# Performance work log

Measured on AMD Instinct MI355X. Metric: run time of the kernel, lower is better.

The kernel has to match this reference:

```python
import jax, jax.numpy as jnp
import numpy as np
from jax import lax

STRIDES = (4, 8, 16, 32, 64)
SIZES = (32, 64, 128, 256, 512)
RATIOS = (0.5, 1.0, 2.0)
IMG_H, IMG_W = 1024, 1024
PRE_NMS = 1000
POST_NMS = 1000
NMS_THRESH = 0.7
BBOX_CLIP = float(np.log(1000.0 / 16.0))
NEG_INF = -1e9


def _cell_anchors(size):
    a = []
    for r in RATIOS:
        w = size * np.sqrt(1.0 / r)
        h = size * np.sqrt(r)
        a.append([-w / 2.0, -h / 2.0, w / 2.0, h / 2.0])
    return np.array(a, np.float32)  # [A,4]


def _level_anchors(H, W, stride, size):
    cell = _cell_anchors(size)  # [A,4]
    ys = np.arange(H, dtype=np.float32) * stride
    xs = np.arange(W, dtype=np.float32) * stride
    yy, xx = np.meshgrid(ys, xs, indexing='ij')  # row-major (H,W)
    shifts = np.stack([xx, yy, xx, yy], axis=-1).reshape(-1, 1, 4)
    return jnp.asarray((shifts + cell[None]).reshape(-1, 4))  # [(H*W*A),4] in (H,W,A) order


def conv2d(x, w, b, pad):
    y = lax.conv_general_dilated(x, w, (1, 1), pad,
                                 dimension_numbers=('NCHW', 'OIHW', 'NCHW'))
    return y + b[None, :, None, None]


def decode(deltas, anchors):
    widths = anchors[:, 2] - anchors[:, 0] + 1.0
    heights = anchors[:, 3] - anchors[:, 1] + 1.0
    ctr_x = anchors[:, 0] + 0.5 * widths
    ctr_y = anchors[:, 1] + 0.5 * heights
    dx, dy = deltas[..., 0], deltas[..., 1]
    dw = jnp.minimum(deltas[..., 2], BBOX_CLIP)
    dh = jnp.minimum(deltas[..., 3], BBOX_CLIP)
    pcx = dx * widths + ctr_x
    pcy = dy * heights + ctr_y
    pw = jnp.exp(dw) * widths
    ph = jnp.exp(dh) * heights
    return jnp.stack([pcx - 0.5 * pw, pcy - 0.5 * ph,
                      pcx + 0.5 * pw - 1.0, pcy + 0.5 * ph - 1.0], axis=-1)


def iou_matrix(boxes):
    area = (boxes[:, 2] - boxes[:, 0]) * (boxes[:, 3] - boxes[:, 1])
    lt = jnp.maximum(boxes[:, None, :2], boxes[None, :, :2])
    rb = jnp.minimum(boxes[:, None, 2:], boxes[None, :, 2:])
    wh = jnp.maximum(rb - lt, 0.0)
    inter = wh[..., 0] * wh[..., 1]
    return inter / (area[:, None] + area[None, :] - inter + 1e-9)


def nms_keep(boxes):
    # boxes [N,4] already sorted by score desc; greedy NMS -> bool keep mask
    N = boxes.shape[0]
    iou = iou_matrix(boxes)

    def body(keep, i):
        row = jnp.take(iou, i, axis=0) > NMS_THRESH
        row = row.at[i].set(False)
        keep = jnp.where(keep[i], keep & ~row, keep)
        return keep, None

    keep, _ = lax.scan(body, jnp.ones((N,), bool), jnp.arange(N))
    return keep


def _forward(feats, conv_w, conv_b, cls_w, cls_b, bbox_w, bbox_b):
    level_boxes, level_scores = [], []
    for lvl, feat in enumerate(feats):
        B, _, H, W = feat.shape
        t = jax.nn.relu(conv2d(feat, conv_w, conv_b, 'SAME'))
        logits = conv2d(t, cls_w, cls_b, 'VALID')    # [B,A,H,W]
        breg = conv2d(t, bbox_w, bbox_b, 'VALID')    # [B,4A,H,W]
        A = logits.shape[1]
        scores = jnp.transpose(logits, (0, 2, 3, 1)).reshape(B, -1)            # (H,W,A)
        deltas = breg.reshape(B, A, 4, H, W).transpose(0, 3, 4, 1, 2).reshape(B, -1, 4)
        anchors = _level_anchors(H, W, STRIDES[lvl], SIZES[lvl])
        boxes = decode(deltas, anchors)  # [B,N,4]
        boxes = jnp.stack([jnp.clip(boxes[..., 0], 0.0, IMG_W - 1.0),
                           jnp.clip(boxes[..., 1], 0.0, IMG_H - 1.0),
                           jnp.clip(boxes[..., 2], 0.0, IMG_W - 1.0),
                           jnp.clip(boxes[..., 3], 0.0, IMG_H - 1.0)], axis=-1)
        k = min(PRE_NMS, scores.shape[1])
        top_s, idx = lax.top_k(scores, k)                                   # [B,k]
        top_b = jnp.take_along_axis(boxes, idx[..., None], axis=1)          # [B,k,4]
        keep = jax.vmap(nms_keep)(top_b)                                    # [B,k] bool
        level_scores.append(jnp.where(keep, top_s, NEG_INF))
        level_boxes.append(top_b)
    all_s = jnp.concatenate(level_scores, axis=1)
    all_b = jnp.concatenate(level_boxes, axis=1)
    fs, fi = lax.top_k(all_s, POST_NMS)                                     # [B,POST]
    fb = jnp.take_along_axis(all_b, fi[..., None], axis=1)                  # [B,POST,4]
    return jnp.concatenate([fb, fs[..., None]], axis=-1)                    # [B,POST,5]


def setup_inputs() -> dict:
    key = jax.random.key(0)
    ks = jax.random.split(key, 8)
    C = 256
    feats = {
        'feat0': jax.random.normal(ks[0], (2, C, 256, 256), jnp.float32),
        'feat1': jax.random.normal(ks[1], (2, C, 128, 128), jnp.float32),
        'feat2': jax.random.normal(ks[2], (2, C, 64, 64), jnp.float32),
        'feat3': jax.random.normal(ks[3], (2, C, 32, 32), jnp.float32),
        'feat4': jax.random.normal(ks[4], (2, C, 16, 16), jnp.float32),
    }
    params = {
        'conv_w': jax.random.normal(ks[5], (C, C, 3, 3), jnp.float32) * 0.01,
        'conv_b': jnp.zeros((C,), jnp.float32),
        'cls_w': jax.random.normal(ks[6], (3, C, 1, 1), jnp.float32) * 0.01,
        'cls_b': jnp.zeros((3,), jnp.float32),
        'bbox_w': jax.random.normal(ks[7], (12, C, 1, 1), jnp.float32) * 0.01,
        'bbox_b': jnp.zeros((12,), jnp.float32),
    }
    return {**feats, **params}


def reference(feat0, feat1, feat2, feat3, feat4, conv_w, conv_b, cls_w, cls_b, bbox_w, bbox_b):
    return _forward([feat0, feat1, feat2, feat3, feat4],
                    conv_w, conv_b, cls_w, cls_b, bbox_w, bbox_b)
```

## Files before the change

### kernel.cpp

```cpp
#include <hip/hip_runtime.h>
#include <cmath>


#define NTOT_PER_IMG 261888
#define ATOT_PER_IMG 4768

__constant__ int c_NLVL[5] = {196608, 49152, 12288, 3072, 768};
__constant__ int c_KLVL[5] = {1000, 1000, 1000, 1000, 768};
__constant__ int c_LOFF[5] = {0, 196608, 245760, 258048, 261120};
__constant__ int c_AOFF[5] = {0, 1000, 2000, 3000, 4000};

struct Anch { float cx1[3]; float cy1[3]; };
struct ConvCfg { Anch an[5]; };

__global__ __launch_bounds__(256) void wtrans(const float* __restrict__ Wsrc,
                                              float* __restrict__ Wt) {
  __shared__ float T[16][17];
  int k0 = blockIdx.x * 16;
  int o0 = blockIdx.y * 16;
  int i = threadIdx.x >> 4, j = threadIdx.x & 15;
  T[i][j] = Wsrc[(size_t)(o0 + i) * 2304 + (k0 + j)];
  __syncthreads();
  Wt[(size_t)(k0 + i) * 256 + (o0 + j)] = T[j][i];
}

__global__ __launch_bounds__(256, 6) void conv_all(
    const float* __restrict__ f0, const float* __restrict__ f1,
    const float* __restrict__ f2, const float* __restrict__ f3,
    const float* __restrict__ f4, const float* __restrict__ Wt,
    const float* __restrict__ convb, const float* __restrict__ clsw,
    const float* __restrict__ clsb, const float* __restrict__ bboxw,
    const float* __restrict__ bboxb, float* __restrict__ scoresOut,
    float4* __restrict__ boxesOut, ConvCfg cfg) {
  __shared__ __align__(16) float sm[4096 + 272];
  float* tl = sm;
  float* Red2 = sm + 4096;

  int b = blockIdx.x;
  const float* feat;
  int lvl, img, gy, bx, H, stride, lvlOff;
  if (b < 8192) {
    lvl = 0; feat = f0; H = 256; stride = 4; lvlOff = 0;
    img = b >> 12; int r = b & 4095; gy = r >> 4; bx = r & 15;
  } else if (b < 10240) {
    lvl = 1; feat = f1; H = 128; stride = 8; lvlOff = 196608;
    int rb = b - 8192; img = rb >> 10; int r = rb & 1023; gy = r >> 3; bx = r & 7;
  } else if (b < 10752) {
    lvl = 2; feat = f2; H = 64; stride = 16; lvlOff = 245760;
    int rb = b - 10240; img = rb >> 8; int r = rb & 255; gy = r >> 2; bx = r & 3;
  } else if (b < 10880) {
    lvl = 3; feat = f3; H = 32; stride = 32; lvlOff = 258048;
    int rb = b - 10752; img = rb >> 6; int r = rb & 63; gy = r >> 1; bx = r & 1;
  } else {
    lvl = 4; feat = f4; H = 16; stride = 64; lvlOff = 261120;
    int rb = b - 10880; img = rb >> 4; gy = rb & 15; bx = 0;
  }
  const int W = H;
  const int x0 = bx * 16;
  const Anch an = cfg.an[lvl];

  const int tid = threadIdx.x;
  const int lane = tid & 63;
  const int wav = __builtin_amdgcn_readfirstlane(tid >> 6);
  const int oc = wav * 64 + lane;

  const float* f = feat + (size_t)img * 256 * H * W;

  float acc[16];
#pragma unroll
  for (int p = 0; p < 16; p++) acc[p] = 0.f;

  const bool leftEdge = (x0 == 0);
  const bool rightEdge = (x0 + 16 >= W);

#pragma unroll 1
  for (int ic = 0; ic < 256; ic++) {
    const float* frow0 = f + (size_t)ic * H * W;
#pragma unroll
    for (int ky = 0; ky < 3; ky++) {
      int row = gy + ky - 1;
      float a[18];
      if (row >= 0 && row < H) {
        const float* rp = frow0 + (size_t)row * W + x0;
#pragma unroll
        for (int j = 0; j < 16; j++) a[j + 1] = rp[j];
        a[0] = leftEdge ? 0.f : rp[-1];
        a[17] = rightEdge ? 0.f : rp[16];
      } else {
#pragma unroll
        for (int j = 0; j < 18; j++) a[j] = 0.f;
      }
      const float* wrow = Wt + (size_t)(ic * 9 + ky * 3) * 256 + oc;
      float w0 = wrow[0];
      float w1 = wrow[256];
      float w2 = wrow[512];
#pragma unroll
      for (int p = 0; p < 16; p++) acc[p] = __builtin_fmaf(w0, a[p], acc[p]);
#pragma unroll
      for (int p = 0; p < 16; p++) acc[p] = __builtin_fmaf(w1, a[p + 1], acc[p]);
#pragma unroll
      for (int p = 0; p < 16; p++) acc[p] = __builtin_fmaf(w2, a[p + 2], acc[p]);
    }
  }

  float cb = convb[oc];
#pragma unroll
  for (int p = 0; p < 16; p++)
    tl[p * 256 + oc] = fmaxf(acc[p] + cb, 0.f);
  __syncthreads();

  if (tid < 240) {
    int px = tid / 15, c = tid - px * 15;
    const float* wr0 = (c < 3) ? (clsw + c * 256) : (bboxw + (c - 3) * 256);
    float bb = (c < 3) ? clsb[c] : bboxb[c - 3];
    const float* trow = &tl[px * 256];
    float tot = 0.f;
#pragma unroll
    for (int g = 0; g < 16; g++) {
      const float* wr = wr0 + g * 16;
      const float* tr = trow + g * 16;
      float s = 0.f;
#pragma unroll
      for (int i = 0; i < 16; i++) s += wr[i] * tr[i];
      tot += s;
    }
    Red2[px * 17 + c] = tot + bb;
  }
  __syncthreads();

  const float BCLIP = (float)4.135166556742356;
  const size_t base = (size_t)img * NTOT_PER_IMG + lvlOff;
  if (tid < 48) {
    int px = tid / 3, a = tid - px * 3;
    int gx = x0 + px;
    float sc = Red2[px * 17 + a];
    float dxv = Red2[px * 17 + 3 + a * 4 + 0];
    float dyv = Red2[px * 17 + 3 + a * 4 + 1];
    float dwv = Red2[px * 17 + 3 + a * 4 + 2];
    float dhv = Red2[px * 17 + 3 + a * 4 + 3];
    float sx = (float)(gx * stride), sy = (float)(gy * stride);
    float x1 = __fadd_rn(sx, an.cx1[a]);
    float x2 = __fsub_rn(sx, an.cx1[a]);
    float y1 = __fadd_rn(sy, an.cy1[a]);
    float y2 = __fsub_rn(sy, an.cy1[a]);
    float wdt = __fadd_rn(__fsub_rn(x2, x1), 1.0f);
    float hgt = __fadd_rn(__fsub_rn(y2, y1), 1.0f);
    float ctx = __fadd_rn(x1, __fmul_rn(0.5f, wdt));
    float cty = __fadd_rn(y1, __fmul_rn(0.5f, hgt));
    float dw = fminf(dwv, BCLIP), dh = fminf(dhv, BCLIP);
    float pcx = __fadd_rn(__fmul_rn(dxv, wdt), ctx);
    float pcy = __fadd_rn(__fmul_rn(dyv, hgt), cty);
    float pw = __fmul_rn(expf(dw), wdt);
    float ph = __fmul_rn(expf(dh), hgt);
    float hw = __fmul_rn(0.5f, pw), hh = __fmul_rn(0.5f, ph);
    float bx1 = __fsub_rn(pcx, hw);
    float by1 = __fsub_rn(pcy, hh);
    float bx2 = __fsub_rn(__fadd_rn(pcx, hw), 1.0f);
    float by2 = __fsub_rn(__fadd_rn(pcy, hh), 1.0f);
    bx1 = fminf(fmaxf(bx1, 0.f), 1023.f);
    by1 = fminf(fmaxf(by1, 0.f), 1023.f);
    bx2 = fminf(fmaxf(bx2, 0.f), 1023.f);
    by2 = fminf(fmaxf(by2, 0.f), 1023.f);
    int g = gy * W + gx;
    size_t o = base + (size_t)g * 3 + a;
    scoresOut[o] = sc;
    boxesOut[o] = make_float4(bx1, by1, bx2, by2);
  }
}

__device__ __forceinline__ unsigned fkey(float f) {
  unsigned b = __float_as_uint(f);
  return (b & 0x80000000u) ? ~b : (b | 0x80000000u);
}
__device__ __forceinline__ float funkey(unsigned u) {
  unsigned b = (u & 0x80000000u) ? (u & 0x7fffffffu) : ~u;
  return __uint_as_float(b);
}

template <bool FINAL>
__global__ __launch_bounds__(1024) void topk_kernel(
    const float* __restrict__ scoresIn, const float4* __restrict__ boxesIn,
    float* __restrict__ scoresOut, float4* __restrict__ boxesOut,
    float* __restrict__ finalOut) {
  __shared__ unsigned long long keys[1024];
  __shared__ unsigned hist[256];
  __shared__ unsigned s_comm[4];
  int lvl = 0, img, N, k;
  const float* src;
  const float4* bsrc;
  if (FINAL) {
    img = blockIdx.x; N = ATOT_PER_IMG; k = 1000;
    src = scoresIn + (size_t)img * ATOT_PER_IMG;
    bsrc = boxesIn + (size_t)img * ATOT_PER_IMG;
  } else {
    lvl = blockIdx.x; img = blockIdx.y;
    N = c_NLVL[lvl]; k = c_KLVL[lvl];
    src = scoresIn + (size_t)img * NTOT_PER_IMG + c_LOFF[lvl];
    bsrc = boxesIn + (size_t)img * NTOT_PER_IMG + c_LOFF[lvl];
  }
  const int tid = threadIdx.x;

  unsigned pref = 0, pmask = 0, krem = (unsigned)k, cntT = 0;
  for (int pass = 3; pass >= 0; pass--) {
    int shift = pass * 8;
    if (tid < 256) hist[tid] = 0;
    __syncthreads();
    for (int i = tid; i < N; i += 1024) {
      unsigned u = fkey(src[i]);
      if ((u & pmask) == pref) atomicAdd(&hist[(u >> shift) & 255], 1u);
    }
    __syncthreads();
    if (tid == 0) {
      unsigned cum = 0;
      for (int d = 255; d >= 0; d--) {
        unsigned c = hist[d];
        if (cum + c >= krem) {
          s_comm[0] = krem - cum; s_comm[1] = c; s_comm[2] = (unsigned)d;
          break;
        }
        cum += c;
      }
    }
    __syncthreads();
    krem = s_comm[0]; cntT = s_comm[1];
    pref |= s_comm[2] << shift;
    pmask |= 0xFFu << shift;
    __syncthreads();
  }
  const unsigned T = pref, r = krem;
  unsigned m = (unsigned)N;
  if (r < cntT) {
    unsigned lo = 0, hi = (unsigned)N;
    while (lo < hi) {
      unsigned mid = (lo + hi) >> 1;
      if (tid == 0) s_comm[3] = 0;
      __syncthreads();
      for (unsigned i = tid; i < mid; i += 1024)
        if (fkey(src[i]) == T) atomicAdd(&s_comm[3], 1u);
      __syncthreads();
      unsigned c = s_comm[3];
      __syncthreads();
      if (c >= r) hi = mid; else lo = mid + 1;
    }
    m = lo;
  }
  if (tid == 0) s_comm[3] = 0;
  __syncthreads();
  for (int i = tid; i < N; i += 1024) {
    unsigned u = fkey(src[i]);
    if (u > T || (u == T && (unsigned)i < m)) {
      unsigned p = atomicAdd(&s_comm[3], 1u);
      if (p < 1024)
        keys[p] = ((unsigned long long)u << 32) | (unsigned)(~(unsigned)i);
    }
  }
  __syncthreads();
  if (tid >= k) keys[tid] = 0ull;
  __syncthreads();
  for (unsigned k2 = 2; k2 <= 1024; k2 <<= 1) {
    for (unsigned j = k2 >> 1; j > 0; j >>= 1) {
      unsigned i = tid, ixj = i ^ j;
      if (ixj > i) {
        unsigned long long a = keys[i], b = keys[ixj];
        bool sw = ((i & k2) == 0) ? (a < b) : (a > b);
        if (sw) { keys[i] = b; keys[ixj] = a; }
      }
      __syncthreads();
    }
  }
  if (tid < k) {
    unsigned long long key = keys[tid];
    unsigned u = (unsigned)(key >> 32);
    unsigned idx = ~((unsigned)key);
    float sc = funkey(u);
    float4 b = bsrc[idx];
    if (FINAL) {
      float* o = finalOut + ((size_t)img * 1000 + tid) * 5;
      o[0] = b.x; o[1] = b.y; o[2] = b.z; o[3] = b.w; o[4] = sc;
    } else {
      scoresOut[(size_t)img * ATOT_PER_IMG + c_AOFF[lvl] + tid] = sc;
      boxesOut[(size_t)img * ATOT_PER_IMG + c_AOFF[lvl] + tid] = b;
    }
  }
}

__global__ __launch_bounds__(256) void nms_matrix(
    const float4* __restrict__ allb, unsigned long long* __restrict__ supp) {
  int lvl = blockIdx.x, img = blockIdx.y, rb = blockIdx.z;
  int k = c_KLVL[lvl];
  int task = img * 5 + lvl;
  const float4* src = allb + (size_t)img * ATOT_PER_IMG + c_AOFF[lvl];
  __shared__ float4 bb[1000];
  __shared__ float ar[1000];
  for (int j = threadIdx.x; j < k; j += 256) {
    float4 b = src[j];
    bb[j] = b;
    ar[j] = __fmul_rn(__fsub_rn(b.z, b.x), __fsub_rn(b.w, b.y));
  }
  __syncthreads();
  int i = rb * 256 + threadIdx.x;
  if (i < k) {
    float4 bi = bb[i];
    float ai = ar[i];
    unsigned long long* row = supp + ((size_t)task * 1024 + i) * 16;
    int jw0 = i >> 6;
    for (int jw = 0; jw < jw0; jw++) row[jw] = 0ull;
    for (int jw = jw0; jw < 16; jw++) {
      unsigned long long bits = 0;
      int jbase = jw * 64;
      for (int jj = 0; jj < 64; jj++) {
        int j = jbase + jj;
        if (j > i && j < k) {
          float4 bj = bb[j];
          float ltx = fmaxf(bi.x, bj.x), lty = fmaxf(bi.y, bj.y);
          float rbx = fminf(bi.z, bj.z), rby = fminf(bi.w, bj.w);
          float wx = fmaxf(__fsub_rn(rbx, ltx), 0.f);
          float wy = fmaxf(__fsub_rn(rby, lty), 0.f);
          float inter = __fmul_rn(wx, wy);
          float den = __fadd_rn(__fsub_rn(__fadd_rn(ai, ar[j]), inter), 1e-9f);
          if (__fdiv_rn(inter, den) > 0.7f) bits |= 1ull << jj;
        }
      }
      row[jw] = bits;
    }
  }
}

__global__ __launch_bounds__(64) void nms_scan(
    const float* __restrict__ topS, const unsigned long long* __restrict__ supp,
    float* __restrict__ fscore) {
  int lvl = blockIdx.x, img = blockIdx.y;
  int k = c_KLVL[lvl];
  int task = img * 5 + lvl;
  int lane = threadIdx.x;
  const unsigned long long* base = supp + (size_t)task * 1024 * 16;
  unsigned long long rem = 0, keep = 0;
  for (int b0 = 0; b0 < k; b0 += 16) {
    unsigned long long buf[16];
#pragma unroll
    for (int t = 0; t < 16; t++) {
      int i = b0 + t;
      buf[t] = (lane < 16 && i < k) ? base[(size_t)i * 16 + lane] : 0ull;
    }
#pragma unroll
    for (int t = 0; t < 16; t++) {
      int i = b0 + t;
      if (i >= k) break;
      int wi = i >> 6, bi = i & 63;
      unsigned long long rw = __shfl(rem, wi);
      if (!((rw >> bi) & 1ull)) {
        rem |= buf[t];
        if (lane == wi) keep |= (1ull << bi);
      }
    }
  }
  const float* ts = topS + (size_t)img * ATOT_PER_IMG + c_AOFF[lvl];
  float* fs = fscore + (size_t)img * ATOT_PER_IMG + c_AOFF[lvl];
  for (int i = lane; i < k; i += 64) {
    int wi = i >> 6;
    unsigned long long kw = __shfl(keep, wi);
    fs[i] = ((kw >> (i & 63)) & 1ull) ? ts[i] : -1e9f;
  }
}

static Anch mkAnch(double size) {
  Anch a;
  const double R[3] = {0.5, 1.0, 2.0};
  for (int i = 0; i < 3; i++) {
    double w = size * sqrt(1.0 / R[i]);
    double h = size * sqrt(R[i]);
    a.cx1[i] = (float)(-w / 2.0);
    a.cy1[i] = (float)(-h / 2.0);
  }
  return a;
}

extern "C" void kernel_launch(void* const* d_in, const int* in_sizes, int n_in,
                              void* d_out, int out_size, void* d_ws,
                              size_t ws_size, hipStream_t stream) {
  (void)in_sizes; (void)n_in; (void)out_size; (void)ws_size;
  const float* f0 = (const float*)d_in[0];
  const float* f1 = (const float*)d_in[1];
  const float* f2 = (const float*)d_in[2];
  const float* f3 = (const float*)d_in[3];
  const float* f4 = (const float*)d_in[4];
  const float* conv_w = (const float*)d_in[5];
  const float* conv_b = (const float*)d_in[6];
  const float* cls_w  = (const float*)d_in[7];
  const float* cls_b  = (const float*)d_in[8];
  const float* bbox_w = (const float*)d_in[9];
  const float* bbox_b = (const float*)d_in[10];
  float* out = (float*)d_out;

  float* wsf = (float*)d_ws;
  float* Wt     = wsf;
  float* scores = Wt + 589824;
  float* boxes  = scores + 2 * NTOT_PER_IMG;
  float* topS   = boxes + (size_t)2 * NTOT_PER_IMG * 4;
  float* allb   = topS + 2 * ATOT_PER_IMG;
  float* fscore = allb + (size_t)2 * ATOT_PER_IMG * 4;
  unsigned long long* supp =
      (unsigned long long*)(fscore + 2 * ATOT_PER_IMG);

  wtrans<<<dim3(144, 16), 256, 0, stream>>>(conv_w, Wt);

  ConvCfg cfg;
  const double SZ[5] = {32, 64, 128, 256, 512};
  for (int l = 0; l < 5; l++) cfg.an[l] = mkAnch(SZ[l]);

  conv_all<<<10912, 256, 0, stream>>>(f0, f1, f2, f3, f4, Wt, conv_b, cls_w,
                                      cls_b, bbox_w, bbox_b, scores,
                                      (float4*)boxes, cfg);

  topk_kernel<false><<<dim3(5, 2), 1024, 0, stream>>>(
      scores, (const float4*)boxes, topS, (float4*)allb, nullptr);
  nms_matrix<<<dim3(5, 2, 4), 256, 0, stream>>>((const float4*)allb, supp);
  nms_scan<<<dim3(5, 2), 64, 0, stream>>>(topS, supp, fscore);
  topk_kernel<true><<<2, 1024, 0, stream>>>(
      fscore, (const float4*)allb, nullptr, nullptr, out);
}
```

Measured before the change: 3.827 ms.

## Compute two output rows per conv block to reuse loaded input rows and weights

Each conv block now produces two adjacent output rows. It loads four input rows per channel instead of three per output row, and loads all nine weights once for both rows, which halves the grid. Out-of-bounds rows are now handled with clamped addresses and bit masks instead of branches. The cost is twice the accumulator registers, which may reduce occupancy under the 6-wave launch bound, and the head/decode epilogue now runs twice per block with extra barriers.

```diff
diff --git a/kernel.cpp b/kernel.cpp
--- a/kernel.cpp
+++ b/kernel.cpp
@@ -38,25 +38,27 @@
 
   int b = blockIdx.x;
   const float* feat;
-  int lvl, img, gy, bx, H, stride, lvlOff;
-  if (b < 8192) {
+  int lvl, img, gy2, bx, H, stride, lvlOff;
+  if (b < 4096) {
     lvl = 0; feat = f0; H = 256; stride = 4; lvlOff = 0;
-    img = b >> 12; int r = b & 4095; gy = r >> 4; bx = r & 15;
-  } else if (b < 10240) {
+    img = b >> 11; int r = b & 2047; gy2 = r >> 4; bx = r & 15;
+  } else if (b < 5120) {
     lvl = 1; feat = f1; H = 128; stride = 8; lvlOff = 196608;
-    int rb = b - 8192; img = rb >> 10; int r = rb & 1023; gy = r >> 3; bx = r & 7;
-  } else if (b < 10752) {
+    int rb = b - 4096; img = rb >> 9; int r = rb & 511; gy2 = r >> 3; bx = r & 7;
+  } else if (b < 5376) {
     lvl = 2; feat = f2; H = 64; stride = 16; lvlOff = 245760;
-    int rb = b - 10240; img = rb >> 8; int r = rb & 255; gy = r >> 2; bx = r & 3;
-  } else if (b < 10880) {
+    int rb = b - 5120; img = rb >> 7; int r = rb & 127; gy2 = r >> 2; bx = r & 3;
+  } else if (b < 5440) {
     lvl = 3; feat = f3; H = 32; stride = 32; lvlOff = 258048;
-    int rb = b - 10752; img = rb >> 6; int r = rb & 63; gy = r >> 1; bx = r & 1;
+    int rb = b - 5376; img = rb >> 5; int r = rb & 31; gy2 = r >> 1; bx = r & 1;
   } else {
     lvl = 4; feat = f4; H = 16; stride = 64; lvlOff = 261120;
-    int rb = b - 10880; img = rb >> 4; gy = rb & 15; bx = 0;
+    int rb = b - 5440; img = rb >> 3; gy2 = rb & 7; bx = 0;
   }
   const int W = H;
+  const int HW = H * W;
   const int x0 = bx * 16;
+  const int gy0 = gy2 * 2;
   const Anch an = cfg.an[lvl];
 
   const int tid = threadIdx.x;
@@ -64,107 +66,135 @@
   const int wav = __builtin_amdgcn_readfirstlane(tid >> 6);
   const int oc = wav * 64 + lane;
 
-  const float* f = feat + (size_t)img * 256 * H * W;
-
-  float acc[16];
-#pragma unroll
-  for (int p = 0; p < 16; p++) acc[p] = 0.f;
+  const float* f = feat + (size_t)img * 256 * HW;
+
+  float acc0[16], acc1[16];
+#pragma unroll
+  for (int p = 0; p < 16; p++) { acc0[p] = 0.f; acc1[p] = 0.f; }
 
   const bool leftEdge = (x0 == 0);
   const bool rightEdge = (x0 + 16 >= W);
+  const unsigned mskL = leftEdge ? 0u : 0xFFFFFFFFu;
+  const unsigned mskR = rightEdge ? 0u : 0xFFFFFFFFu;
+  const int offL = leftEdge ? 0 : -1;
+  const int offR = rightEdge ? 15 : 16;
+
+#define LOADROW(arr, rowi)                                                   \
+  {                                                                          \
+    int row_ = (rowi);                                                       \
+    unsigned msk_ = (row_ >= 0 && row_ < H) ? 0xFFFFFFFFu : 0u;              \
+    int rc_ = row_ < 0 ? 0 : (row_ >= H ? H - 1 : row_);                     \
+    const float* rp_ = pl + (size_t)rc_ * W + x0;                            \
+    arr[0] = __uint_as_float(__float_as_uint(rp_[offL]) & msk_ & mskL);      \
+    _Pragma("unroll")                                                        \
+    for (int j_ = 0; j_ < 16; j_++)                                          \
+      arr[j_ + 1] = __uint_as_float(__float_as_uint(rp_[j_]) & msk_);        \
+    arr[17] = __uint_as_float(__float_as_uint(rp_[offR]) & msk_ & mskR);     \
+  }
+
+#define FMA3(accA, arr, w0_, w1_, w2_)                                       \
+  {                                                                          \
+    _Pragma("unroll")                                                        \
+    for (int p_ = 0; p_ < 16; p_++)                                          \
+      accA[p_] = __builtin_fmaf(w0_, arr[p_], accA[p_]);                     \
+    _Pragma("unroll")                                                        \
+    for (int p_ = 0; p_ < 16; p_++)                                          \
+      accA[p_] = __builtin_fmaf(w1_, arr[p_ + 1], accA[p_]);                 \
+    _Pragma("unroll")                                                        \
+    for (int p_ = 0; p_ < 16; p_++)                                          \
+      accA[p_] = __builtin_fmaf(w2_, arr[p_ + 2], accA[p_]);                 \
+  }
 
 #pragma unroll 1
   for (int ic = 0; ic < 256; ic++) {
-    const float* frow0 = f + (size_t)ic * H * W;
-#pragma unroll
-    for (int ky = 0; ky < 3; ky++) {
-      int row = gy + ky - 1;
-      float a[18];
-      if (row >= 0 && row < H) {
-        const float* rp = frow0 + (size_t)row * W + x0;
-#pragma unroll
-        for (int j = 0; j < 16; j++) a[j + 1] = rp[j];
-        a[0] = leftEdge ? 0.f : rp[-1];
-        a[17] = rightEdge ? 0.f : rp[16];
-      } else {
-#pragma unroll
-        for (int j = 0; j < 18; j++) a[j] = 0.f;
-      }
-      const float* wrow = Wt + (size_t)(ic * 9 + ky * 3) * 256 + oc;
-      float w0 = wrow[0];
-      float w1 = wrow[256];
-      float w2 = wrow[512];
-#pragma unroll
-      for (int p = 0; p < 16; p++) acc[p] = __builtin_fmaf(w0, a[p], acc[p]);
-#pragma unroll
-      for (int p = 0; p < 16; p++) acc[p] = __builtin_fmaf(w1, a[p + 1], acc[p]);
-#pragma unroll
-      for (int p = 0; p < 16; p++) acc[p] = __builtin_fmaf(w2, a[p + 2], acc[p]);
-    }
-  }
-
-  float cb = convb[oc];
-#pragma unroll
-  for (int p = 0; p < 16; p++)
-    tl[p * 256 + oc] = fmaxf(acc[p] + cb, 0.f);
-  __syncthreads();
-
-  if (tid < 240) {
-    int px = tid / 15, c = tid - px * 15;
-    const float* wr0 = (c < 3) ? (clsw + c * 256) : (bboxw + (c - 3) * 256);
-    float bb = (c < 3) ? clsb[c] : bboxb[c - 3];
-    const float* trow = &tl[px * 256];
-    float tot = 0.f;
-#pragma unroll
-    for (int g = 0; g < 16; g++) {
-      const float* wr = wr0 + g * 16;
-      const float* tr = trow + g * 16;
-      float s = 0.f;
-#pragma unroll
-      for (int i = 0; i < 16; i++) s += wr[i] * tr[i];
-      tot += s;
-    }
-    Red2[px * 17 + c] = tot + bb;
-  }
-  __syncthreads();
-
+    const float* pl = f + (size_t)ic * HW;
+    const float* wrow = Wt + (size_t)ic * 9 * 256 + oc;
+    float w00 = wrow[0 * 256], w01 = wrow[1 * 256], w02 = wrow[2 * 256];
+    float w10 = wrow[3 * 256], w11 = wrow[4 * 256], w12 = wrow[5 * 256];
+    float w20 = wrow[6 * 256], w21 = wrow[7 * 256], w22 = wrow[8 * 256];
+    float R0[18], R1[18], R2[18], R3[18];
+    LOADROW(R0, gy0 - 1)
+    LOADROW(R1, gy0)
+    LOADROW(R2, gy0 + 1)
+    LOADROW(R3, gy0 + 2)
+    FMA3(acc0, R0, w00, w01, w02)
+    FMA3(acc1, R1, w00, w01, w02)
+    FMA3(acc0, R1, w10, w11, w12)
+    FMA3(acc1, R2, w10, w11, w12)
+    FMA3(acc0, R2, w20, w21, w22)
+    FMA3(acc1, R3, w20, w21, w22)
+  }
+#undef LOADROW
+#undef FMA3
+
+  const float cb = convb[oc];
   const float BCLIP = (float)4.135166556742356;
   const size_t base = (size_t)img * NTOT_PER_IMG + lvlOff;
-  if (tid < 48) {
-    int px = tid / 3, a = tid - px * 3;
-    int gx = x0 + px;
-    float sc = Red2[px * 17 + a];
-    float dxv = Red2[px * 17 + 3 + a * 4 + 0];
-    float dyv = Red2[px * 17 + 3 + a * 4 + 1];
-    float dwv = Red2[px * 17 + 3 + a * 4 + 2];
-    float dhv = Red2[px * 17 + 3 + a * 4 + 3];
-    float sx = (float)(gx * stride), sy = (float)(gy * stride);
-    float x1 = __fadd_rn(sx, an.cx1[a]);
-    float x2 = __fsub_rn(sx, an.cx1[a]);
-    float y1 = __fadd_rn(sy, an.cy1[a]);
-    float y2 = __fsub_rn(sy, an.cy1[a]);
-    float wdt = __fadd_rn(__fsub_rn(x2, x1), 1.0f);
-    float hgt = __fadd_rn(__fsub_rn(y2, y1), 1.0f);
-    float ctx = __fadd_rn(x1, __fmul_rn(0.5f, wdt));
-    float cty = __fadd_rn(y1, __fmul_rn(0.5f, hgt));
-    float dw = fminf(dwv, BCLIP), dh = fminf(dhv, BCLIP);
-    float pcx = __fadd_rn(__fmul_rn(dxv, wdt), ctx);
-    float pcy = __fadd_rn(__fmul_rn(dyv, hgt), cty);
-    float pw = __fmul_rn(expf(dw), wdt);
-    float ph = __fmul_rn(expf(dh), hgt);
-    float hw = __fmul_rn(0.5f, pw), hh = __fmul_rn(0.5f, ph);
-    float bx1 = __fsub_rn(pcx, hw);
-    float by1 = __fsub_rn(pcy, hh);
-    float bx2 = __fsub_rn(__fadd_rn(pcx, hw), 1.0f);
-    float by2 = __fsub_rn(__fadd_rn(pcy, hh), 1.0f);
-    bx1 = fminf(fmaxf(bx1, 0.f), 1023.f);
-    by1 = fminf(fmaxf(by1, 0.f), 1023.f);
-    bx2 = fminf(fmaxf(bx2, 0.f), 1023.f);
-    by2 = fminf(fmaxf(by2, 0.f), 1023.f);
-    int g = gy * W + gx;
-    size_t o = base + (size_t)g * 3 + a;
-    scoresOut[o] = sc;
-    boxesOut[o] = make_float4(bx1, by1, bx2, by2);
+
+#pragma unroll
+  for (int rr = 0; rr < 2; rr++) {
+    const int gy = gy0 + rr;
+#pragma unroll
+    for (int p = 0; p < 16; p++)
+      tl[p * 256 + oc] = fmaxf((rr ? acc1[p] : acc0[p]) + cb, 0.f);
+    __syncthreads();
+
+    if (tid < 240) {
+      int px = tid / 15, c = tid - px * 15;
+      const float* wr0 = (c < 3) ? (clsw + c * 256) : (bboxw + (c - 3) * 256);
+      float bb = (c < 3) ? clsb[c] : bboxb[c - 3];
+      const float* trow = &tl[px * 256];
+      float tot = 0.f;
+#pragma unroll
+      for (int g = 0; g < 16; g++) {
+        const float* wr = wr0 + g * 16;
+        const float* tr = trow + g * 16;
+        float s = 0.f;
+#pragma unroll
+        for (int i = 0; i < 16; i++) s += wr[i] * tr[i];
+        tot += s;
+      }
+      Red2[px * 17 + c] = tot + bb;
+    }
+    __syncthreads();
+
+    if (tid < 48) {
+      int px = tid / 3, a = tid - px * 3;
+      int gx = x0 + px;
+      float sc = Red2[px * 17 + a];
+      float dxv = Red2[px * 17 + 3 + a * 4 + 0];
+      float dyv = Red2[px * 17 + 3 + a * 4 + 1];
+      float dwv = Red2[px * 17 + 3 + a * 4 + 2];
+      float dhv = Red2[px * 17 + 3 + a * 4 + 3];
+      float sx = (float)(gx * stride), sy = (float)(gy * stride);
+      float x1 = __fadd_rn(sx, an.cx1[a]);
+      float x2 = __fsub_rn(sx, an.cx1[a]);
+      float y1 = __fadd_rn(sy, an.cy1[a]);
+      float y2 = __fsub_rn(sy, an.cy1[a]);
+      float wdt = __fadd_rn(__fsub_rn(x2, x1), 1.0f);
+      float hgt = __fadd_rn(__fsub_rn(y2, y1), 1.0f);
+      float ctx = __fadd_rn(x1, __fmul_rn(0.5f, wdt));
+      float cty = __fadd_rn(y1, __fmul_rn(0.5f, hgt));
+      float dw = fminf(dwv, BCLIP), dh = fminf(dhv, BCLIP);
+      float pcx = __fadd_rn(__fmul_rn(dxv, wdt), ctx);
+      float pcy = __fadd_rn(__fmul_rn(dyv, hgt), cty);
+      float pw = __fmul_rn(expf(dw), wdt);
+      float ph = __fmul_rn(expf(dh), hgt);
+      float hw = __fmul_rn(0.5f, pw), hh = __fmul_rn(0.5f, ph);
+      float bx1 = __fsub_rn(pcx, hw);
+      float by1 = __fsub_rn(pcy, hh);
+      float bx2 = __fsub_rn(__fadd_rn(pcx, hw), 1.0f);
+      float by2 = __fsub_rn(__fadd_rn(pcy, hh), 1.0f);
+      bx1 = fminf(fmaxf(bx1, 0.f), 1023.f);
+      by1 = fminf(fmaxf(by1, 0.f), 1023.f);
+      bx2 = fminf(fmaxf(bx2, 0.f), 1023.f);
+      by2 = fminf(fmaxf(by2, 0.f), 1023.f);
+      int g = gy * W + gx;
+      size_t o = base + (size_t)g * 3 + a;
+      scoresOut[o] = sc;
+      boxesOut[o] = make_float4(bx1, by1, bx2, by2);
+    }
+    __syncthreads();
   }
 }
 
@@ -408,9 +438,9 @@
   const double SZ[5] = {32, 64, 128, 256, 512};
   for (int l = 0; l < 5; l++) cfg.an[l] = mkAnch(SZ[l]);
 
-  conv_all<<<10912, 256, 0, stream>>>(f0, f1, f2, f3, f4, Wt, conv_b, cls_w,
-                                      cls_b, bbox_w, bbox_b, scores,
-                                      (float4*)boxes, cfg);
+  conv_all<<<5456, 256, 0, stream>>>(f0, f1, f2, f3, f4, Wt, conv_b, cls_w,
+                                     cls_b, bbox_w, bbox_b, scores,
+                                     (float4*)boxes, cfg);
 
   topk_kernel<false><<<dim3(5, 2), 1024, 0, stream>>>(
       scores, (const float4*)boxes, topS, (float4*)allb, nullptr);
```

New measurement: 4.670 ms. 22.0% more time.
